# Optimization experiments

Hardware: AMD Instinct MI355X
Metric: run time of the kernel (lower is better)

The kernel has to match this reference:

```python
import jax, jax.numpy as jnp
import numpy as np
import math

B, S, E = 4, 2048, 1024

def setup_inputs() -> dict:
    key = jax.random.key(0)
    ks = jax.random.split(key, 12)
    scale = 1.0 / math.sqrt(E)
    inp = {
        "query": jax.random.normal(ks[0], (B, S, E), jnp.float32),
        "key_": jax.random.normal(ks[1], (B, S, E), jnp.float32),
        "value": jax.random.normal(ks[2], (B, S, E), jnp.float32),
        # causal mask, broadcast over batch: 1 = keep, 0 = mask
        "mask": jnp.broadcast_to(jnp.tril(jnp.ones((S, S), jnp.int32)), (B, S, S)),
        "Wq": jax.random.uniform(ks[3], (E, E), jnp.float32, -scale, scale),
        "bq": jax.random.uniform(ks[4], (E,), jnp.float32, -scale, scale),
        "Wk": jax.random.uniform(ks[5], (E, E), jnp.float32, -scale, scale),
        "bk": jax.random.uniform(ks[6], (E,), jnp.float32, -scale, scale),
        "Wv": jax.random.uniform(ks[7], (E, E), jnp.float32, -scale, scale),
        "bv": jax.random.uniform(ks[8], (E,), jnp.float32, -scale, scale),
        "Wo": jax.random.uniform(ks[9], (E, E), jnp.float32, -scale, scale),
        "bo": jax.random.uniform(ks[10], (E,), jnp.float32, -scale, scale),
    }
    return inp

def reference(query, key_, value, mask, Wq, bq, Wk, bk, Wv, bv, Wo, bo):
    # Linear projections (torch Linear: x @ W.T + b)
    Q = jnp.einsum('bse,fe->bsf', query, Wq) + bq
    K = jnp.einsum('bse,fe->bsf', key_, Wk) + bk
    V = jnp.einsum('bse,fe->bsf', value, Wv) + bv
    # NOTE: module never splits heads; scores over full embed_dim, scaled by sqrt(embed_dim)
    scores = jnp.einsum('bqe,bke->bqk', Q, K) / jnp.sqrt(jnp.asarray(E, Q.dtype))
    scores = jnp.where(mask == 0, -jnp.inf, scores)
    attn = jax.nn.softmax(scores, axis=-1)
    attn_out = jnp.einsum('bqk,bke->bqe', attn, V)
    return jnp.einsum('bse,fe->bsf', attn_out, Wo) + bo
```

## Files before the change

kernel.cpp:

```cpp
#include <hip/hip_runtime.h>

typedef __bf16 bf16;
typedef __attribute__((ext_vector_type(8))) __bf16 bf16x8;
typedef __attribute__((ext_vector_type(4))) __bf16 bf16x4;
typedef __attribute__((ext_vector_type(4))) float f32x4;

#define DEVINL __device__ __forceinline__

DEVINL void gload_lds16(const bf16* g, bf16* l) {
    __builtin_amdgcn_global_load_lds(
        (__attribute__((address_space(1))) unsigned int*)(unsigned long long)g,
        (__attribute__((address_space(3))) unsigned int*)l,
        16, 0, 0);
}

__global__ __launch_bounds__(256) void cvt3_f32_to_bf16(
    const float* __restrict__ a, const float* __restrict__ b,
    const float* __restrict__ c, bf16* __restrict__ out, int n4) {
    int i = blockIdx.x * blockDim.x + threadIdx.x;
    if (i >= n4) return;
    const float* src = (blockIdx.z == 0) ? a : (blockIdx.z == 1) ? b : c;
    bf16* dst = out + (size_t)blockIdx.z * (size_t)n4 * 4;
    float4 f = ((const float4*)src)[i];
    bf16x4 o;
    o.x = (bf16)f.x; o.y = (bf16)f.y; o.z = (bf16)f.z; o.w = (bf16)f.w;
    ((bf16x4*)dst)[i] = o;
}

__global__ __launch_bounds__(256) void cvt4_f32_to_bf16(
    const float* __restrict__ a, const float* __restrict__ b,
    const float* __restrict__ c, const float* __restrict__ d,
    bf16* __restrict__ out, int n4) {
    int i = blockIdx.x * blockDim.x + threadIdx.x;
    if (i >= n4) return;
    const float* src = (blockIdx.z == 0) ? a : (blockIdx.z == 1) ? b
                     : (blockIdx.z == 2) ? c : d;
    bf16* dst = out + (size_t)blockIdx.z * (size_t)n4 * 4;
    float4 f = ((const float4*)src)[i];
    bf16x4 o;
    o.x = (bf16)f.x; o.y = (bf16)f.y; o.z = (bf16)f.z; o.w = (bf16)f.w;
    ((bf16x4*)dst)[i] = o;
}

__global__ __launch_bounds__(256) void transpose_bf16(
    const unsigned short* __restrict__ in, unsigned short* __restrict__ out,
    int R, int C) {
    __shared__ unsigned short t[64][65];
    const size_t bo = (size_t)blockIdx.z * R * C;
    const int r0 = blockIdx.y * 64, c0 = blockIdx.x * 64;
#pragma unroll
    for (int i = 0; i < 16; i++) {
        int lin = threadIdx.x + i * 256;
        int r = lin >> 6, c = lin & 63;
        t[r][c] = in[bo + (size_t)(r0 + r) * C + (c0 + c)];
    }
    __syncthreads();
#pragma unroll
    for (int i = 0; i < 16; i++) {
        int lin = threadIdx.x + i * 256;
        int r = lin >> 6, c = lin & 63;
        out[bo + (size_t)(c0 + r) * R + (r0 + c)] = t[c][r];
    }
}

template <int EPI>
__global__ __launch_bounds__(256) void gemm_bt(
    const bf16* __restrict__ A, const bf16* __restrict__ B,
    const float* __restrict__ bias, void* __restrict__ Cv,
    int M, int N, int K,
    long long sA, long long sB, long long sC, long long sBias,
    float scale, int causal) {
    const int bx = blockIdx.x, by = blockIdx.y, bz = blockIdx.z;
    const int m0 = by * 128, n0 = bx * 64;
    if (causal == 1 && n0 > m0 + 127) return;
    int Keff = K;
    if (causal == 2) { Keff = m0 + 128; if (Keff > K) Keff = K; }

    A += (size_t)bz * sA;
    B += (size_t)bz * sB;
    if (bias) bias += (size_t)bz * sBias;

    __shared__ __align__(16) bf16 As[128 * 32];
    __shared__ __align__(16) bf16 Bs[64 * 32];

    const int tid = threadIdx.x;
    const int wave = tid >> 6;
    const int lane = tid & 63;
    const int lr = lane & 15;
    const int lq = lane >> 4;
    const int wm = wave * 32;

    const int srow = lane >> 2;
    const int scol = (lane & 3) * 8;

    f32x4 acc[2][4];
    const f32x4 fzero = {0.f, 0.f, 0.f, 0.f};
#pragma unroll
    for (int i = 0; i < 2; i++)
#pragma unroll
        for (int j = 0; j < 4; j++) acc[i][j] = fzero;

    for (int k0 = 0; k0 < Keff; k0 += 32) {
        const bf16* ga0 = A + (size_t)(m0 + wave * 16 + srow) * K + (k0 + scol);
        const bf16* gb0 = B + (size_t)(n0 + wave * 16 + srow) * K + (k0 + scol);
        gload_lds16(ga0,                  As + wave * 512);
        gload_lds16(ga0 + (size_t)64 * K, As + (wave + 4) * 512);
        gload_lds16(gb0,                  Bs + wave * 512);
        __syncthreads();

        bf16x8 af[2], bfr[4];
#pragma unroll
        for (int i = 0; i < 2; i++)
            af[i] = *(const bf16x8*)(As + (wm + i * 16 + lr) * 32 + lq * 8);
#pragma unroll
        for (int j = 0; j < 4; j++)
            bfr[j] = *(const bf16x8*)(Bs + (j * 16 + lr) * 32 + lq * 8);
#pragma unroll
        for (int i = 0; i < 2; i++)
#pragma unroll
            for (int j = 0; j < 4; j++)
                acc[i][j] = __builtin_amdgcn_mfma_f32_16x16x32_bf16(
                    af[i], bfr[j], acc[i][j], 0, 0, 0);
        __syncthreads();
    }

    if (EPI == 0) {
        bf16* C = (bf16*)Cv + (size_t)bz * sC;
#pragma unroll
        for (int j = 0; j < 4; j++) {
            const int col = n0 + j * 16 + lr;
            const float bb = bias ? bias[col] : 0.0f;
#pragma unroll
            for (int i = 0; i < 2; i++) {
                const int rowb = m0 + wm + i * 16 + lq * 4;
#pragma unroll
                for (int r = 0; r < 4; r++)
                    C[(size_t)(rowb + r) * N + col] =
                        (bf16)(acc[i][j][r] * scale + bb);
            }
        }
    } else {
        float* C = (float*)Cv + (size_t)bz * sC;
#pragma unroll
        for (int j = 0; j < 4; j++) {
            const int col = n0 + j * 16 + lr;
            const float bb = bias ? bias[col] : 0.0f;
#pragma unroll
            for (int i = 0; i < 2; i++) {
                const int rowb = m0 + wm + i * 16 + lq * 4;
#pragma unroll
                for (int r = 0; r < 4; r++)
                    C[(size_t)(rowb + r) * N + col] =
                        acc[i][j][r] * scale + bb;
            }
        }
    }
}

__global__ __launch_bounds__(256) void softmax_causal(
    const float* __restrict__ Sc, bf16* __restrict__ P, int S) {
    const int row = blockIdx.x;
    const int q = row & (S - 1);
    const float* src = Sc + (size_t)row * S;
    bf16* dst = P + (size_t)row * S;
    const int L = q + 1;
    const int tid = threadIdx.x;

    float v[8];
    float mx = -3.0e38f;
#pragma unroll
    for (int i = 0; i < 8; i++) {
        int k = tid + i * 256;
        v[i] = (k < L) ? src[k] : -3.0e38f;
        mx = fmaxf(mx, v[i]);
    }
#pragma unroll
    for (int off = 32; off > 0; off >>= 1) mx = fmaxf(mx, __shfl_xor(mx, off, 64));
    __shared__ float redm[4], reds[4];
    if ((tid & 63) == 0) redm[tid >> 6] = mx;
    __syncthreads();
    mx = fmaxf(fmaxf(redm[0], redm[1]), fmaxf(redm[2], redm[3]));

    float sum = 0.f;
#pragma unroll
    for (int i = 0; i < 8; i++) {
        int k = tid + i * 256;
        float e = (k < L) ? __expf(v[i] - mx) : 0.f;
        v[i] = e;
        sum += e;
    }
#pragma unroll
    for (int off = 32; off > 0; off >>= 1) sum += __shfl_xor(sum, off, 64);
    if ((tid & 63) == 0) reds[tid >> 6] = sum;
    __syncthreads();
    sum = reds[0] + reds[1] + reds[2] + reds[3];
    const float inv = 1.0f / sum;
#pragma unroll
    for (int i = 0; i < 8; i++) {
        int k = tid + i * 256;
        dst[k] = (bf16)(v[i] * inv);
    }
}

extern "C" void kernel_launch(void* const* d_in, const int* in_sizes, int n_in,
                              void* d_out, int out_size, void* d_ws, size_t ws_size,
                              hipStream_t stream) {
    const int B = 4, S = 2048, E = 1024;
    const size_t SBE = (size_t)B * S * E;
    const size_t EE = (size_t)E * E;

    const float* q_in = (const float*)d_in[0];
    const float* k_in = (const float*)d_in[1];
    const float* v_in = (const float*)d_in[2];
    const float* Wq = (const float*)d_in[4];
    const float* bq = (const float*)d_in[5];
    const float* Wk = (const float*)d_in[6];
    const float* bk = (const float*)d_in[7];
    const float* Wv = (const float*)d_in[8];
    const float* bv = (const float*)d_in[9];
    const float* Wo = (const float*)d_in[10];
    const float* bo = (const float*)d_in[11];

    char* ws = (char*)d_ws;
    bf16* qkvb = (bf16*)ws;
    float* Sc = (float*)ws;
    bf16* AO = (bf16*)ws;
    char* p = ws + (size_t)B * S * S * 4;
    bf16* QKVb = (bf16*)p; p += 3 * SBE * 2;
    bf16* Vt = (bf16*)p; p += SBE * 2;
    bf16* Pb = (bf16*)p; p += (size_t)B * S * S * 2;
    bf16* Wb = (bf16*)p; p += 4 * EE * 2;
    float* biasWS = (float*)p; p += 3 * E * 4;

    bf16* Qb = QKVb;
    bf16* Vb = QKVb + 2 * SBE;
    bf16* Wob = Wb + 3 * EE;

    dim3 gcvt3((int)(SBE / 4 / 256), 1, 3);
    cvt3_f32_to_bf16<<<gcvt3, 256, 0, stream>>>(q_in, k_in, v_in, qkvb, (int)(SBE / 4));
    dim3 gcvt4((int)(EE / 4 / 256), 1, 4);
    cvt4_f32_to_bf16<<<gcvt4, 256, 0, stream>>>(Wq, Wk, Wv, Wo, Wb, (int)(EE / 4));
    hipMemcpyAsync(biasWS,         bq, E * 4, hipMemcpyDeviceToDevice, stream);
    hipMemcpyAsync(biasWS + E,     bk, E * 4, hipMemcpyDeviceToDevice, stream);
    hipMemcpyAsync(biasWS + 2 * E, bv, E * 4, hipMemcpyDeviceToDevice, stream);

    dim3 blk(256);
    dim3 gproj(E / 64, (B * S) / 128, 3);
    gemm_bt<0><<<gproj, blk, 0, stream>>>(qkvb, Wb, biasWS, QKVb,
                                          B * S, E, E,
                                          (long long)SBE, (long long)EE,
                                          (long long)SBE, (long long)E, 1.f, 0);

    dim3 gt(E / 64, S / 64, B);
    transpose_bf16<<<gt, blk, 0, stream>>>((const unsigned short*)Vb,
                                           (unsigned short*)Vt, S, E);

    dim3 gsc(S / 64, S / 128, B);
    gemm_bt<1><<<gsc, blk, 0, stream>>>(Qb, QKVb + SBE, nullptr, Sc, S, S, E,
                                        (long long)S * E, (long long)S * E,
                                        (long long)S * S, 0, 0.03125f, 1);

    softmax_causal<<<B * S, 256, 0, stream>>>(Sc, Pb, S);

    dim3 gpv(E / 64, S / 128, B);
    gemm_bt<0><<<gpv, blk, 0, stream>>>(Pb, Vt, nullptr, AO, S, E, S,
                                        (long long)S * S, (long long)E * S,
                                        (long long)S * E, 0, 1.f, 2);

    dim3 gout(E / 64, (B * S) / 128, 1);
    gemm_bt<1><<<gout, blk, 0, stream>>>(AO, Wob, bo, (float*)d_out,
                                         B * S, E, E, 0, 0, 0, 0, 1.f, 0);
}
```

Baseline: 451.8 us.

## Add 128x128 GEMM tile for QKV projection and double K-step in 64-wide GEMM

```diff
diff --git a/kernel.cpp b/kernel.cpp
--- a/kernel.cpp
+++ b/kernel.cpp
@@ -64,7 +64,86 @@
 }
 
 template <int EPI>
-__global__ __launch_bounds__(256) void gemm_bt(
+__global__ __launch_bounds__(256) void gemm_bt128(
+    const bf16* __restrict__ A, const bf16* __restrict__ B,
+    const float* __restrict__ bias, void* __restrict__ Cv,
+    int M, int N, int K,
+    long long sA, long long sB, long long sC, long long sBias,
+    float scale) {
+    const int bx = blockIdx.x, by = blockIdx.y, bz = blockIdx.z;
+    const int m0 = by * 128, n0 = bx * 128;
+
+    A += (size_t)bz * sA;
+    B += (size_t)bz * sB;
+    if (bias) bias += (size_t)bz * sBias;
+
+    __shared__ __align__(16) bf16 As[128 * 32];
+    __shared__ __align__(16) bf16 Bs[128 * 32];
+
+    const int tid = threadIdx.x;
+    const int wave = tid >> 6;
+    const int lane = tid & 63;
+    const int lr = lane & 15;
+    const int lq = lane >> 4;
+    const int wm = (wave >> 1) * 64;
+    const int wn = (wave & 1) * 64;
+    const int srow = lane >> 2;
+    const int scol = (lane & 3) * 8;
+
+    f32x4 acc[4][4];
+    const f32x4 fzero = {0.f, 0.f, 0.f, 0.f};
+#pragma unroll
+    for (int i = 0; i < 4; i++)
+#pragma unroll
+        for (int j = 0; j < 4; j++) acc[i][j] = fzero;
+
+    for (int k0 = 0; k0 < K; k0 += 32) {
+        const bf16* ga0 = A + (size_t)(m0 + wave * 16 + srow) * K + (k0 + scol);
+        const bf16* gb0 = B + (size_t)(n0 + wave * 16 + srow) * K + (k0 + scol);
+        gload_lds16(ga0,                  As + wave * 512);
+        gload_lds16(ga0 + (size_t)64 * K, As + (wave + 4) * 512);
+        gload_lds16(gb0,                  Bs + wave * 512);
+        gload_lds16(gb0 + (size_t)64 * K, Bs + (wave + 4) * 512);
+        __syncthreads();
+
+        bf16x8 af[4], bfr[4];
+#pragma unroll
+        for (int i = 0; i < 4; i++)
+            af[i] = *(const bf16x8*)(As + (wm + i * 16 + lr) * 32 + lq * 8);
+#pragma unroll
+        for (int j = 0; j < 4; j++)
+            bfr[j] = *(const bf16x8*)(Bs + (wn + j * 16 + lr) * 32 + lq * 8);
+#pragma unroll
+        for (int i = 0; i < 4; i++)
+#pragma unroll
+            for (int j = 0; j < 4; j++)
+                acc[i][j] = __builtin_amdgcn_mfma_f32_16x16x32_bf16(
+                    af[i], bfr[j], acc[i][j], 0, 0, 0);
+        __syncthreads();
+    }
+
+#pragma unroll
+    for (int j = 0; j < 4; j++) {
+        const int col = n0 + wn + j * 16 + lr;
+        const float bb = bias ? bias[col] : 0.0f;
+#pragma unroll
+        for (int i = 0; i < 4; i++) {
+            const int rowb = m0 + wm + i * 16 + lq * 4;
+#pragma unroll
+            for (int r = 0; r < 4; r++) {
+                if (EPI == 0)
+                    ((bf16*)Cv)[(size_t)bz * sC + (size_t)(rowb + r) * N + col] =
+                        (bf16)(acc[i][j][r] * scale + bb);
+                else
+                    ((float*)Cv)[(size_t)bz * sC + (size_t)(rowb + r) * N + col] =
+                        acc[i][j][r] * scale + bb;
+            }
+        }
+    }
+}
+
+template <int EPI>
+__global__ __launch_bounds__(256) void gemm_bt64(
     const bf16* __restrict__ A, const bf16* __restrict__ B,
     const float* __restrict__ bias, void* __restrict__ Cv,
     int M, int N, int K,
@@ -80,8 +159,8 @@
     B += (size_t)bz * sB;
     if (bias) bias += (size_t)bz * sBias;
 
-    __shared__ __align__(16) bf16 As[128 * 32];
-    __shared__ __align__(16) bf16 Bs[64 * 32];
+    __shared__ __align__(16) bf16 As[2][128 * 32];
+    __shared__ __align__(16) bf16 Bs[2][64 * 32];
 
     const int tid = threadIdx.x;
     const int wave = tid >> 6;
@@ -89,7 +168,6 @@
     const int lr = lane & 15;
     const int lq = lane >> 4;
     const int wm = wave * 32;
-
     const int srow = lane >> 2;
     const int scol = (lane & 3) * 8;
 
@@ -100,57 +178,54 @@
 #pragma unroll
         for (int j = 0; j < 4; j++) acc[i][j] = fzero;
 
-    for (int k0 = 0; k0 < Keff; k0 += 32) {
-        const bf16* ga0 = A + (size_t)(m0 + wave * 16 + srow) * K + (k0 + scol);
-        const bf16* gb0 = B + (size_t)(n0 + wave * 16 + srow) * K + (k0 + scol);
-        gload_lds16(ga0,                  As + wave * 512);
-        gload_lds16(ga0 + (size_t)64 * K, As + (wave + 4) * 512);
-        gload_lds16(gb0,                  Bs + wave * 512);
+    for (int k0 = 0; k0 < Keff; k0 += 64) {
+#pragma unroll
+        for (int kc = 0; kc < 2; kc++) {
+            const bf16* ga0 =
+                A + (size_t)(m0 + wave * 16 + srow) * K + (k0 + kc * 32 + scol);
+            const bf16* gb0 =
+                B + (size_t)(n0 + wave * 16 + srow) * K + (k0 + kc * 32 + scol);
+            gload_lds16(ga0,                  As[kc] + wave * 512);
+            gload_lds16(ga0 + (size_t)64 * K, As[kc] + (wave + 4) * 512);
+            gload_lds16(gb0,                  Bs[kc] + wave * 512);
+        }
         __syncthreads();
 
-        bf16x8 af[2], bfr[4];
-#pragma unroll
-        for (int i = 0; i < 2; i++)
-            af[i] = *(const bf16x8*)(As + (wm + i * 16 + lr) * 32 + lq * 8);
-#pragma unroll
-        for (int j = 0; j < 4; j++)
-            bfr[j] = *(const bf16x8*)(Bs + (j * 16 + lr) * 32 + lq * 8);
-#pragma unroll
-        for (int i = 0; i < 2; i++)
+        bf16x8 af[2][2], bfr[2][4];
+#pragma unroll
+        for (int kc = 0; kc < 2; kc++) {
+#pragma unroll
+            for (int i = 0; i < 2; i++)
+                af[kc][i] = *(const bf16x8*)(As[kc] + (wm + i * 16 + lr) * 32 + lq * 8);
 #pragma unroll
             for (int j = 0; j < 4; j++)
-                acc[i][j] = __builtin_amdgcn_mfma_f32_16x16x32_bf16(
-                    af[i], bfr[j], acc[i][j], 0, 0, 0);
+                bfr[kc][j] = *(const bf16x8*)(Bs[kc] + (j * 16 + lr) * 32 + lq * 8);
+        }
+#pragma unroll
+        for (int kc = 0; kc < 2; kc++)
+#pragma unroll
+            for (int i = 0; i < 2; i++)
+#pragma unroll
+                for (int j = 0; j < 4; j++)
+                    acc[i][j] = __builtin_amdgcn_mfma_f32_16x16x32_bf16(
+                        af[kc][i], bfr[kc][j], acc[i][j], 0, 0, 0);
         __syncthreads();
     }
 
-    if (EPI == 0) {
-        bf16* C = (bf16*)Cv + (size_t)bz * sC;
-#pragma unroll
-        for (int j = 0; j < 4; j++) {
-            const int col = n0 + j * 16 + lr;
-            const float bb = bias ? bias[col] : 0.0f;
-#pragma unroll
-            for (int i = 0; i < 2; i++) {
-                const int rowb = m0 + wm + i * 16 + lq * 4;
-#pragma unroll
-                for (int r = 0; r < 4; r++)
-                    C[(size_t)(rowb + r) * N + col] =
+#pragma unroll
+    for (int j = 0; j < 4; j++) {
+        const int col = n0 + j * 16 + lr;
+        const float bb = bias ? bias[col] : 0.0f;
+#pragma unroll
+        for (int i = 0; i < 2; i++) {
+            const int rowb = m0 + wm + i * 16 + lq * 4;
+#pragma unroll
+            for (int r = 0; r < 4; r++) {
+                if (EPI == 0)
+                    ((bf16*)Cv)[(size_t)bz * sC + (size_t)(rowb + r) * N + col] =
                         (bf16)(acc[i][j][r] * scale + bb);
-            }
-        }
-    } else {
-        float* C = (float*)Cv + (size_t)bz * sC;
-#pragma unroll
-        for (int j = 0; j < 4; j++) {
-            const int col = n0 + j * 16 + lr;
-            const float bb = bias ? bias[col] : 0.0f;
-#pragma unroll
-            for (int i = 0; i < 2; i++) {
-                const int rowb = m0 + wm + i * 16 + lq * 4;
-#pragma unroll
-                for (int r = 0; r < 4; r++)
-                    C[(size_t)(rowb + r) * N + col] =
+                else
+                    ((float*)Cv)[(size_t)bz * sC + (size_t)(rowb + r) * N + col] =
                         acc[i][j][r] * scale + bb;
             }
         }
@@ -245,29 +320,29 @@
     hipMemcpyAsync(biasWS + 2 * E, bv, E * 4, hipMemcpyDeviceToDevice, stream);
 
     dim3 blk(256);
-    dim3 gproj(E / 64, (B * S) / 128, 3);
-    gemm_bt<0><<<gproj, blk, 0, stream>>>(qkvb, Wb, biasWS, QKVb,
-                                          B * S, E, E,
-                                          (long long)SBE, (long long)EE,
-                                          (long long)SBE, (long long)E, 1.f, 0);
+    dim3 gproj(E / 128, (B * S) / 128, 3);
+    gemm_bt128<0><<<gproj, blk, 0, stream>>>(qkvb, Wb, biasWS, QKVb,
+                                             B * S, E, E,
+                                             (long long)SBE, (long long)EE,
+                                             (long long)SBE, (long long)E, 1.f);
 
     dim3 gt(E / 64, S / 64, B);
     transpose_bf16<<<gt, blk, 0, stream>>>((const unsigned short*)Vb,
                                            (unsigned short*)Vt, S, E);
 
     dim3 gsc(S / 64, S / 128, B);
-    gemm_bt<1><<<gsc, blk, 0, stream>>>(Qb, QKVb + SBE, nullptr, Sc, S, S, E,
-                                        (long long)S * E, (long long)S * E,
-                                        (long long)S * S, 0, 0.03125f, 1);
+    gemm_bt64<1><<<gsc, blk, 0, stream>>>(Qb, QKVb + SBE, nullptr, Sc, S, S, E,
+                                          (long long)S * E, (long long)S * E,
+                                          (long long)S * S, 0, 0.03125f, 1);
 
     softmax_causal<<<B * S, 256, 0, stream>>>(Sc, Pb, S);
 
     dim3 gpv(E / 64, S / 128, B);
-    gemm_bt<0><<<gpv, blk, 0, stream>>>(Pb, Vt, nullptr, AO, S, E, S,
-                                        (long long)S * S, (long long)E * S,
-                                        (long long)S * E, 0, 1.f, 2);
+    gemm_bt64<0><<<gpv, blk, 0, stream>>>(Pb, Vt, nullptr, AO, S, E, S,
+                                          (long long)S * S, (long long)E * S,
+                                          (long long)S * E, 0, 1.f, 2);
 
     dim3 gout(E / 64, (B * S) / 128, 1);
-    gemm_bt<1><<<gout, blk, 0, stream>>>(AO, Wob, bo, (float*)d_out,
-                                         B * S, E, E, 0, 0, 0, 0, 1.f, 0);
-}
+    gemm_bt64<1><<<gout, blk, 0, stream>>>(AO, Wob, bo, (float*)d_out,
+                                           B * S, E, E, 0, 0, 0, 0, 1.f, 0);
+}
```

Result: faster. 431.7 us (-4.4%).
